# Performance work log

Hardware: AMD Instinct MI355X
Metric: run time of the kernel (lower is better)

## Reference

```python
import jax, jax.numpy as jnp
import numpy as np
import math

IN_FEATURES = 512
KERNEL = 3
EPS = 1e-08
GAIN = 1.0 / math.sqrt(IN_FEATURES * KERNEL * KERNEL)  # lr_multiplier=1


def setup_inputs() -> dict:
    key = jax.random.key(0)
    k1, k2, k3 = jax.random.split(key, 3)
    x = jax.random.normal(k1, (16, 512, 32, 32), dtype=jnp.float32)
    style = jax.random.normal(k2, (16, 512), dtype=jnp.float32)
    weight = jax.random.normal(k3, (512, 512, 3, 3), dtype=jnp.float32)
    return {"x": x, "style": style, "weight": weight}


def reference(x, style, weight):
    # w: [B, O, I, k, k] = gain-scaled weight modulated per-sample by style over input channels
    w = (weight * GAIN)[None] * style[:, None, :, None, None]
    # demodulate: rsqrt of sum of squares over (I, kh, kw) per (B, O)
    sigma = jax.lax.rsqrt(jnp.sum(jnp.square(w), axis=(2, 3, 4)) + EPS)
    w = w * sigma[:, :, None, None, None]
    # per-sample conv2d with padding='same' (stride 1, k=3 -> pad 1)
    def conv_one(xi, wi):  # xi: [C,H,W], wi: [O,I,k,k]
        return jax.lax.conv_general_dilated(
            xi[None], wi, window_strides=(1, 1), padding='SAME',
            dimension_numbers=('NCHW', 'OIHW', 'NCHW'))[0]
    return jax.vmap(conv_one)(x, w)  # [B, O, H, W]
```

## Files before the change

kernel.cpp:

```cpp
#include <hip/hip_runtime.h>
#include <hip/hip_bf16.h>

#define EPSF 1e-8f
#define GAINF 0.014731391274719739f

typedef __attribute__((ext_vector_type(8))) __bf16 bf16x8;
typedef __attribute__((ext_vector_type(4))) __bf16 bf16x4;
typedef __attribute__((ext_vector_type(16))) float f32x16;

#define GLOAD_LDS16(gp, lp) __builtin_amdgcn_global_load_lds( \
    (const __attribute__((address_space(1))) unsigned int*)(gp), \
    (__attribute__((address_space(3))) unsigned int*)(lp), 16, 0, 0)

__global__ void k_prep(const float* __restrict__ x, const float* __restrict__ style,
                       const float* __restrict__ w, float* __restrict__ S,
                       __hip_bfloat16* __restrict__ wbf, __hip_bfloat16* __restrict__ xs) {
  int blk = blockIdx.x, tid = threadIdx.x;
  if (blk < 2048) {
    __shared__ float tile[64][65];
    int b = blk >> 7, rem = blk & 127, ct = rem >> 4, pt = rem & 15;
    int p0 = pt * 64, c0 = ct * 64;
    int tx = tid & 63, ty = tid >> 6;
#pragma unroll
    for (int k = 0; k < 16; ++k) {
      int ci = ty + k * 4;
      tile[ci][tx] = x[((b * 512) + (c0 + ci)) * 1024 + p0 + tx];
    }
    __syncthreads();
    int tq = tid & 15, py = tid >> 4;
    int c = c0 + tq * 4;
    int cb = c >> 5, cw = c & 31;
    float st0 = style[b * 512 + c], st1 = style[b * 512 + c + 1];
    float st2 = style[b * 512 + c + 2], st3 = style[b * 512 + c + 3];
#pragma unroll
    for (int k = 0; k < 4; ++k) {
      int pl = py + k * 16;
      int p = p0 + pl;
      int y = p >> 5, xx = p & 31;
      int site = (y + 1) * 34 + (xx + 1);
      bf16x4 v;
      v[0] = (__bf16)(tile[tq * 4 + 0][pl] * st0);
      v[1] = (__bf16)(tile[tq * 4 + 1][pl] * st1);
      v[2] = (__bf16)(tile[tq * 4 + 2][pl] * st2);
      v[3] = (__bf16)(tile[tq * 4 + 3][pl] * st3);
      *reinterpret_cast<bf16x4*>(xs + (size_t)(((b * 16 + cb) * 1156 + site) * 32 + cw)) = v;
    }
  } else if (blk < 3072) {
    int idx = (blk - 2048) * 256 + tid;
    int o = idx >> 9, i = idx & 511;
    const float* p = w + (size_t)idx * 9;
    float s = 0.f;
#pragma unroll
    for (int t = 0; t < 9; ++t) {
      float v = p[t];
      s += v * v;
      wbf[(size_t)t * 262144 + (i >> 5) * 16384 + o * 32 + (i & 31)] = __float2bfloat16(v);
    }
    S[idx] = s;
  } else {
    int bb = blk - 3072;
    int b = bb >> 4, cb = bb & 15;
    for (int i2 = tid; i2 < 528; i2 += 256) {
      int sb = i2 >> 2, q = i2 & 3;
      int yp, xp;
      if (sb < 34) { yp = 0; xp = sb; }
      else if (sb < 68) { yp = 33; xp = sb - 34; }
      else { int t2 = sb - 68; yp = 1 + (t2 >> 1); xp = (t2 & 1) * 33; }
      float4 z = {0.f, 0.f, 0.f, 0.f};
      *reinterpret_cast<float4*>(xs + (size_t)(((b * 16 + cb) * 1156 + yp * 34 + xp) * 32 + q * 8)) = z;
    }
  }
}

__global__ void k_sigma(const float* __restrict__ style, const float* __restrict__ S,
                        float* __restrict__ esc) {
  __shared__ float s2[8192];
  __shared__ float red[4][16];
  int tid = threadIdx.x, o = blockIdx.x;
  for (int idx = tid; idx < 8192; idx += 256) {
    float v = style[idx];
    s2[idx] = v * v;
  }
  __syncthreads();
  float acc[16];
#pragma unroll
  for (int b = 0; b < 16; ++b) acc[b] = 0.f;
  for (int i = tid; i < 512; i += 256) {
    float s = S[o * 512 + i];
#pragma unroll
    for (int b = 0; b < 16; ++b) acc[b] += s2[b * 512 + i] * s;
  }
#pragma unroll
  for (int b = 0; b < 16; ++b)
#pragma unroll
    for (int off = 32; off; off >>= 1) acc[b] += __shfl_down(acc[b], off);
  int lane = tid & 63, wv = tid >> 6;
  if (lane == 0)
#pragma unroll
    for (int b = 0; b < 16; ++b) red[wv][b] = acc[b];
  __syncthreads();
  if (tid < 16) {
    float s = red[0][tid] + red[1][tid] + red[2][tid] + red[3][tid];
    esc[tid * 512 + o] = GAINF * rsqrtf(s * (GAINF * GAINF) + EPSF);
  }
}

__global__ __launch_bounds__(256, 2) void k_conv(
    const __hip_bfloat16* __restrict__ wbf, const __hip_bfloat16* __restrict__ xs,
    const float* __restrict__ esc, float* __restrict__ out) {
  __shared__ __hip_bfloat16 ldsB[2 * 4352];
  int g = blockIdx.x;
  int xcd = g & 7, sblk = g >> 3;
  int mg = sblk >> 5;
  int n = xcd * 32 + (sblk & 31);
  int b = n >> 4, nt = n & 15;
  int row0 = nt * 2;
  int tid = threadIdx.x;
  int wv = tid >> 6, lane = tid & 63;
  int l31 = lane & 31, lhi = lane >> 5;
  int o_base = mg * 256 + wv * 64;

  int roff[3];
#pragma unroll
  for (int j = 0; j < 3; ++j) {
    int idx = wv * 136 + j * 64 + lane;
    int site = idx >> 2, q0 = idx & 3;
    int qs = q0 ^ ((site >> 1) & 3);
    roff[j] = site * 32 + qs * 8;
  }

#define STAGE(cbv) do { \
    const __hip_bfloat16* _g = xs + (size_t)((b * 16 + (cbv)) * 1156 + row0 * 34) * 32; \
    __hip_bfloat16* _l = ldsB + ((cbv) & 1) * 4352 + wv * 1088 + lane * 8; \
    _Pragma("unroll") \
    for (int _j = 0; _j < 2; ++_j) GLOAD_LDS16(_g + roff[_j], _l + _j * 512); \
    if (lane < 8) GLOAD_LDS16(_g + roff[2], _l + 2 * 512); \
  } while (0)

  int wrow = (o_base + l31) * 32 + lhi * 8;
#define LOADA(dst, t_, cb_) do { \
    const __hip_bfloat16* _p = wbf + (size_t)(t_) * 262144 + (cb_) * 16384 + wrow; \
    dst[0][0] = *reinterpret_cast<const bf16x8*>(_p); \
    dst[1][0] = *reinterpret_cast<const bf16x8*>(_p + 16); \
    dst[0][1] = *reinterpret_cast<const bf16x8*>(_p + 1024); \
    dst[1][1] = *reinterpret_cast<const bf16x8*>(_p + 1024 + 16); \
  } while (0)

  f32x16 acc[2][2];
#pragma unroll
  for (int i = 0; i < 2; ++i)
#pragma unroll
    for (int j = 0; j < 2; ++j)
#pragma unroll
      for (int e = 0; e < 16; ++e) acc[i][j][e] = 0.f;

  bf16x8 aC[2][2], aN[2][2];
  STAGE(0);
  LOADA(aC, 0, 0);

  for (int cb = 0; cb < 16; ++cb) {
    __syncthreads();
    if (cb < 15) STAGE(cb + 1);
    const __hip_bfloat16* lb = ldsB + (cb & 1) * 4352;
#pragma unroll
    for (int t = 0; t < 9; ++t) {
      const int dy = t / 3, dx = t - dy * 3;
      if (cb < 15 || t < 8) {
        int tn = (t == 8) ? 0 : t + 1;
        int cbn = (t == 8) ? cb + 1 : cb;
        LOADA(aN, tn, cbn);
      }
      int s[2], sw[2];
#pragma unroll
      for (int ns = 0; ns < 2; ++ns) {
        s[ns] = (ns + dy) * 34 + l31 + dx;
        sw[ns] = (s[ns] >> 1) & 3;
      }
#pragma unroll
      for (int k2 = 0; k2 < 2; ++k2) {
        int ko = (k2 << 1) | lhi;
        bf16x8 bf[2];
#pragma unroll
        for (int ns = 0; ns < 2; ++ns)
          bf[ns] = *reinterpret_cast<const bf16x8*>(&lb[(s[ns] * 4 + (ko ^ sw[ns])) * 8]);
#pragma unroll
        for (int ns = 0; ns < 2; ++ns) {
          acc[0][ns] = __builtin_amdgcn_mfma_f32_32x32x16_bf16(aC[k2][0], bf[ns], acc[0][ns], 0, 0, 0);
          acc[1][ns] = __builtin_amdgcn_mfma_f32_32x32x16_bf16(aC[k2][1], bf[ns], acc[1][ns], 0, 0, 0);
        }
      }
#pragma unroll
      for (int k2 = 0; k2 < 2; ++k2) {
        aC[k2][0] = aN[k2][0];
        aC[k2][1] = aN[k2][1];
      }
    }
  }
  int pxb = nt * 64 + l31;
#pragma unroll
  for (int ms = 0; ms < 2; ++ms)
#pragma unroll
    for (int reg = 0; reg < 16; ++reg) {
      int o = o_base + ms * 32 + (reg & 3) + ((reg >> 2) << 3) + (lhi << 2);
      float e = esc[(b << 9) + o];
#pragma unroll
      for (int ns = 0; ns < 2; ++ns)
        out[(size_t)((b << 9) + o) * 1024 + pxb + ns * 32] = acc[ms][ns][reg] * e;
    }
#undef STAGE
#undef LOADA
}

extern "C" void kernel_launch(void* const* d_in, const int* in_sizes, int n_in,
                              void* d_out, int out_size, void* d_ws, size_t ws_size,
                              hipStream_t stream) {
  const float* x = (const float*)d_in[0];
  const float* style = (const float*)d_in[1];
  const float* w = (const float*)d_in[2];
  float* out = (float*)d_out;
  char* ws = (char*)d_ws;
  __hip_bfloat16* wbf = (__hip_bfloat16*)(ws);
  __hip_bfloat16* xs  = (__hip_bfloat16*)(ws + 4718592);
  float* S   = (float*)(ws + 23658496);
  float* esc = (float*)(ws + 24707072);

  hipLaunchKernelGGL(k_prep, dim3(3328), dim3(256), 0, stream, x, style, w, S, wbf, xs);
  hipLaunchKernelGGL(k_sigma, dim3(512), dim3(256), 0, stream, style, S, esc);
  hipLaunchKernelGGL(k_conv, dim3(512), dim3(256), 0, stream, wbf, xs, esc, out);
}
```

Before: 185.6 us.

## Fuse sigma reduction into prep kernel and deepen weight prefetch to two taps

Merges the separate sigma-computation kernel into the weight-conversion branch of the prep kernel. Each block now handles one output channel, computing the sum of squares and the style-weighted reduction directly, which removes one launch and the round trip through the S buffer. In the conv kernel, the register prefetch of A-operand weights becomes a three-deep rotating queue, loading two taps ahead to hide global-load latency. The deeper queue raises VGPR pressure, and the weight blocks now use 512 larger blocks instead of 1024 smaller ones.

```diff
diff --git a/kernel.cpp b/kernel.cpp
--- a/kernel.cpp
+++ b/kernel.cpp
@@ -13,8 +13,9 @@
     (__attribute__((address_space(3))) unsigned int*)(lp), 16, 0, 0)
 
 __global__ void k_prep(const float* __restrict__ x, const float* __restrict__ style,
-                       const float* __restrict__ w, float* __restrict__ S,
-                       __hip_bfloat16* __restrict__ wbf, __hip_bfloat16* __restrict__ xs) {
+                       const float* __restrict__ w,
+                       __hip_bfloat16* __restrict__ wbf, __hip_bfloat16* __restrict__ xs,
+                       float* __restrict__ esc) {
   int blk = blockIdx.x, tid = threadIdx.x;
   if (blk < 2048) {
     __shared__ float tile[64][65];
@@ -45,20 +46,44 @@
       v[3] = (__bf16)(tile[tq * 4 + 3][pl] * st3);
       *reinterpret_cast<bf16x4*>(xs + (size_t)(((b * 16 + cb) * 1156 + site) * 32 + cw)) = v;
     }
-  } else if (blk < 3072) {
-    int idx = (blk - 2048) * 256 + tid;
-    int o = idx >> 9, i = idx & 511;
-    const float* p = w + (size_t)idx * 9;
-    float s = 0.f;
-#pragma unroll
-    for (int t = 0; t < 9; ++t) {
-      float v = p[t];
-      s += v * v;
-      wbf[(size_t)t * 262144 + (i >> 5) * 16384 + o * 32 + (i & 31)] = __float2bfloat16(v);
-    }
-    S[idx] = s;
+  } else if (blk < 2560) {
+    __shared__ float red[4][16];
+    int o = blk - 2048;
+    float pacc[16];
+#pragma unroll
+    for (int b = 0; b < 16; ++b) pacc[b] = 0.f;
+#pragma unroll
+    for (int half = 0; half < 2; ++half) {
+      int i = tid + half * 256;
+      const float* p = w + (size_t)(o * 512 + i) * 9;
+      float s = 0.f;
+#pragma unroll
+      for (int t = 0; t < 9; ++t) {
+        float v = p[t];
+        s += v * v;
+        wbf[(size_t)t * 262144 + (i >> 5) * 16384 + o * 32 + (i & 31)] = __float2bfloat16(v);
+      }
+#pragma unroll
+      for (int b = 0; b < 16; ++b) {
+        float st = style[b * 512 + i];
+        pacc[b] += st * st * s;
+      }
+    }
+#pragma unroll
+    for (int b = 0; b < 16; ++b)
+#pragma unroll
+      for (int off = 32; off; off >>= 1) pacc[b] += __shfl_down(pacc[b], off);
+    int lane = tid & 63, wv2 = tid >> 6;
+    if (lane == 0)
+#pragma unroll
+      for (int b = 0; b < 16; ++b) red[wv2][b] = pacc[b];
+    __syncthreads();
+    if (tid < 16) {
+      float s = red[0][tid] + red[1][tid] + red[2][tid] + red[3][tid];
+      esc[tid * 512 + o] = GAINF * rsqrtf(s * (GAINF * GAINF) + EPSF);
+    }
   } else {
-    int bb = blk - 3072;
+    int bb = blk - 2560;
     int b = bb >> 4, cb = bb & 15;
     for (int i2 = tid; i2 < 528; i2 += 256) {
       int sb = i2 >> 2, q = i2 & 3;
@@ -69,39 +94,6 @@
       float4 z = {0.f, 0.f, 0.f, 0.f};
       *reinterpret_cast<float4*>(xs + (size_t)(((b * 16 + cb) * 1156 + yp * 34 + xp) * 32 + q * 8)) = z;
     }
-  }
-}
-
-__global__ void k_sigma(const float* __restrict__ style, const float* __restrict__ S,
-                        float* __restrict__ esc) {
-  __shared__ float s2[8192];
-  __shared__ float red[4][16];
-  int tid = threadIdx.x, o = blockIdx.x;
-  for (int idx = tid; idx < 8192; idx += 256) {
-    float v = style[idx];
-    s2[idx] = v * v;
-  }
-  __syncthreads();
-  float acc[16];
-#pragma unroll
-  for (int b = 0; b < 16; ++b) acc[b] = 0.f;
-  for (int i = tid; i < 512; i += 256) {
-    float s = S[o * 512 + i];
-#pragma unroll
-    for (int b = 0; b < 16; ++b) acc[b] += s2[b * 512 + i] * s;
-  }
-#pragma unroll
-  for (int b = 0; b < 16; ++b)
-#pragma unroll
-    for (int off = 32; off; off >>= 1) acc[b] += __shfl_down(acc[b], off);
-  int lane = tid & 63, wv = tid >> 6;
-  if (lane == 0)
-#pragma unroll
-    for (int b = 0; b < 16; ++b) red[wv][b] = acc[b];
-  __syncthreads();
-  if (tid < 16) {
-    float s = red[0][tid] + red[1][tid] + red[2][tid] + red[3][tid];
-    esc[tid * 512 + o] = GAINF * rsqrtf(s * (GAINF * GAINF) + EPSF);
   }
 }
 
@@ -154,9 +146,10 @@
 #pragma unroll
       for (int e = 0; e < 16; ++e) acc[i][j][e] = 0.f;
 
-  bf16x8 aC[2][2], aN[2][2];
+  bf16x8 aQ0[2][2], aQ1[2][2], aQ2[2][2];
   STAGE(0);
-  LOADA(aC, 0, 0);
+  LOADA(aQ0, 0, 0);
+  LOADA(aQ1, 1, 0);
 
   for (int cb = 0; cb < 16; ++cb) {
     __syncthreads();
@@ -165,10 +158,11 @@
 #pragma unroll
     for (int t = 0; t < 9; ++t) {
       const int dy = t / 3, dx = t - dy * 3;
-      if (cb < 15 || t < 8) {
-        int tn = (t == 8) ? 0 : t + 1;
-        int cbn = (t == 8) ? cb + 1 : cb;
-        LOADA(aN, tn, cbn);
+      {
+        const int t2 = t + 2;
+        const int tn = (t2 >= 9) ? t2 - 9 : t2;
+        int cbn = (t2 >= 9) ? cb + 1 : cb;
+        if (cbn < 16) LOADA(aQ2, tn, cbn);
       }
       int s[2], sw[2];
 #pragma unroll
@@ -185,15 +179,17 @@
           bf[ns] = *reinterpret_cast<const bf16x8*>(&lb[(s[ns] * 4 + (ko ^ sw[ns])) * 8]);
 #pragma unroll
         for (int ns = 0; ns < 2; ++ns) {
-          acc[0][ns] = __builtin_amdgcn_mfma_f32_32x32x16_bf16(aC[k2][0], bf[ns], acc[0][ns], 0, 0, 0);
-          acc[1][ns] = __builtin_amdgcn_mfma_f32_32x32x16_bf16(aC[k2][1], bf[ns], acc[1][ns], 0, 0, 0);
+          acc[0][ns] = __builtin_amdgcn_mfma_f32_32x32x16_bf16(aQ0[k2][0], bf[ns], acc[0][ns], 0, 0, 0);
+          acc[1][ns] = __builtin_amdgcn_mfma_f32_32x32x16_bf16(aQ0[k2][1], bf[ns], acc[1][ns], 0, 0, 0);
         }
       }
 #pragma unroll
-      for (int k2 = 0; k2 < 2; ++k2) {
-        aC[k2][0] = aN[k2][0];
-        aC[k2][1] = aN[k2][1];
-      }
+      for (int k2 = 0; k2 < 2; ++k2)
+#pragma unroll
+        for (int ms = 0; ms < 2; ++ms) {
+          aQ0[k2][ms] = aQ1[k2][ms];
+          aQ1[k2][ms] = aQ2[k2][ms];
+        }
     }
   }
   int pxb = nt * 64 + l31;
@@ -221,10 +217,8 @@
   char* ws = (char*)d_ws;
   __hip_bfloat16* wbf = (__hip_bfloat16*)(ws);
   __hip_bfloat16* xs  = (__hip_bfloat16*)(ws + 4718592);
-  float* S   = (float*)(ws + 23658496);
-  float* esc = (float*)(ws + 24707072);
-
-  hipLaunchKernelGGL(k_prep, dim3(3328), dim3(256), 0, stream, x, style, w, S, wbf, xs);
-  hipLaunchKernelGGL(k_sigma, dim3(512), dim3(256), 0, stream, style, S, esc);
+  float* esc = (float*)(ws + 23658496);
+
+  hipLaunchKernelGGL(k_prep, dim3(2816), dim3(256), 0, stream, x, style, w, wbf, xs, esc);
   hipLaunchKernelGGL(k_conv, dim3(512), dim3(256), 0, stream, wbf, xs, esc, out);
 }
```

New measurement: 171.1 us. 1.08x faster.
